# Optimization experiments

Measured on AMD Instinct MI355X. Metric: run time of the kernel, lower is better.

The kernel has to match this reference:

```python
import jax, jax.numpy as jnp
from jax import lax
import numpy as np

B, L, M, D, K, STRIDE = 32, 32768, 32, 128, 16, 8


def setup_inputs() -> dict:
    key = jax.random.key(0)
    k1, k2, k3, k4 = jax.random.split(key, 4)
    x = jax.random.normal(k1, (B, L, M), dtype=jnp.float32)
    # sorted timestamps per sample, like torch.sort(rand*100)
    timestamps = jnp.sort(jax.random.uniform(k2, (B, L), dtype=jnp.float32) * 100.0, axis=1)
    fan_in = M * K
    bound = 1.0 / np.sqrt(fan_in)
    conv_w = jax.random.uniform(k3, (D, M, K), dtype=jnp.float32, minval=-bound, maxval=bound)
    conv_b = jax.random.uniform(k4, (D,), dtype=jnp.float32, minval=-bound, maxval=bound)
    return {"x": x, "timestamps": timestamps, "conv_w": conv_w, "conv_b": conv_b}


def reference(x, timestamps, conv_w, conv_b):
    # Conv1d patch embedding: x [B,L,M] -> NCL -> conv -> [B,P,D]
    patches = lax.conv_general_dilated(
        x.transpose(0, 2, 1), conv_w,
        window_strides=(STRIDE,), padding=[(0, 0)],
        dimension_numbers=("NCH", "OIH", "NCH"))
    patches = patches.transpose(0, 2, 1) + conv_b  # [B,P,D]
    P = patches.shape[1]

    # Per-patch median timestamp (padding=0 -> all windows full length K).
    # torch.median on even-length returns the LOWER median = sorted idx (K-1)//2.
    starts = jnp.arange(P) * STRIDE
    idx = starts[:, None] + jnp.arange(K)          # [P,K]
    windows = timestamps[:, idx]                   # [B,P,K]
    med = jnp.sort(windows, axis=-1)[..., (K - 1) // 2]  # [B,P]

    # Sinusoidal PE at continuous times.
    div_term = jnp.exp(jnp.arange(0, D, 2).astype(jnp.float32) * (-np.log(10000.0) / D))
    ang = med[..., None] * div_term                # [B,P,D//2]
    pe = jnp.stack([jnp.sin(ang), jnp.cos(ang)], axis=-1).reshape(med.shape[0], P, D)
    return patches + pe
```

## Files before the change

kernel.cpp:

```cpp
#include <hip/hip_runtime.h>
#include <hip/hip_bf16.h>

#define Bn 32
#define Ln 32768
#define Mn 32
#define Dn 128
#define Pn 4095
#define KKn 512

typedef short  bf16x8 __attribute__((ext_vector_type(8)));
typedef float  f32x4  __attribute__((ext_vector_type(4)));

union BU { bf16x8 v; unsigned short u[8]; };

static __device__ __forceinline__ unsigned short f2bf(float f) {
  __hip_bfloat16 h = __float2bfloat16(f);
  return *reinterpret_cast<unsigned short*>(&h);
}

static __device__ __forceinline__ int swz(int g) {
  return (g & ~7) | ((g & 7) ^ ((g >> 5) & 7));
}

__global__ __launch_bounds__(256) void prep_w_kernel(const float* __restrict__ w,
                                                     unsigned short* __restrict__ wswz) {
  int idx = blockIdx.x * 256 + threadIdx.x;
  int j = idx & 7;
  int d = (idx >> 3) & 127;
  int g = idx >> 10;
  int kk = g * 8 + j;
  int k = kk >> 5;
  int m = kk & 31;
  wswz[idx] = f2bf(w[(d << 9) + (m << 4) + k]);
}

__global__ __launch_bounds__(256, 4) void gemm_pe_kernel(
    const float* __restrict__ x,
    const float* __restrict__ ts,
    const unsigned short* __restrict__ wswz,
    const float* __restrict__ bias,
    float* __restrict__ out) {

  __shared__ unsigned short xs[2080 * 8];
  __shared__ float tsl[64];

  const int b   = blockIdx.y;
  const int pt0 = blockIdx.x;
  const int tid = threadIdx.x;
  const int lane = tid & 63;
  const int wv   = tid >> 6;
  const int mrow = lane & 15;
  const int quad = lane >> 4;

  const float* xsrc = x + (size_t)b * Ln * Mn + (size_t)pt0 * 512 * Mn;
  const int r0 = pt0 * 512;

  float4 f[8][2];
  #pragma unroll
  for (int i = 0; i < 8; ++i) {
    int g = i * 256 + tid;
    const float4* src = reinterpret_cast<const float4*>(xsrc) + (size_t)g * 2;
    f[i][0] = src[0];
    f[i][1] = src[1];
  }
  float4 t0 = make_float4(0.f, 0.f, 0.f, 0.f), t1 = t0;
  if (tid < 32 && pt0 < 63) {
    const float4* src = reinterpret_cast<const float4*>(xsrc) + (size_t)(2048 + tid) * 2;
    t0 = src[0];
    t1 = src[1];
  }
  float tsv = 0.f;
  if (tid >= 64 && tid < 128)
    tsv = ts[(size_t)b * Ln + r0 + (tid - 64) * 8 + 7];
  const unsigned short* bbase = wswz + (((quad << 7) + (wv << 5) + mrow) << 3);
  bf16x8 bp[3][2];
  #pragma unroll
  for (int j = 0; j < 3; ++j) {
    bp[j][0] = *reinterpret_cast<const bf16x8*>(bbase + j * 4096);
    bp[j][1] = *reinterpret_cast<const bf16x8*>(bbase + 128 + j * 4096);
  }
  const int d0 = wv * 32 + mrow;
  const float NEG_C = -0.14391156831212810f;
  const float div0 = __expf(NEG_C * (float)(d0 >> 1));
  const float div1 = __expf(NEG_C * (float)((d0 + 16) >> 1));
  const float phs  = (d0 & 1) ? 1.5707963267948966f : 0.0f;
  const float bias0 = bias[d0];
  const float bias1 = bias[d0 + 16];

  __builtin_amdgcn_sched_barrier(0);

  #pragma unroll
  for (int i = 0; i < 8; ++i) {
    int g = i * 256 + tid;
    BU bu;
    bu.u[0] = f2bf(f[i][0].x); bu.u[1] = f2bf(f[i][0].y);
    bu.u[2] = f2bf(f[i][0].z); bu.u[3] = f2bf(f[i][0].w);
    bu.u[4] = f2bf(f[i][1].x); bu.u[5] = f2bf(f[i][1].y);
    bu.u[6] = f2bf(f[i][1].z); bu.u[7] = f2bf(f[i][1].w);
    *reinterpret_cast<bf16x8*>(&xs[swz(g) * 8]) = bu.v;
  }
  if (tid < 32) {
    BU bu;
    bu.u[0] = f2bf(t0.x); bu.u[1] = f2bf(t0.y); bu.u[2] = f2bf(t0.z); bu.u[3] = f2bf(t0.w);
    bu.u[4] = f2bf(t1.x); bu.u[5] = f2bf(t1.y); bu.u[6] = f2bf(t1.z); bu.u[7] = f2bf(t1.w);
    *reinterpret_cast<bf16x8*>(&xs[swz(2048 + tid) * 8]) = bu.v;
  }
  if (tid >= 64 && tid < 128) tsl[tid - 64] = tsv;
  __syncthreads();

  int agbase[4];
  #pragma unroll
  for (int pt = 0; pt < 4; ++pt) agbase[pt] = (pt * 16 + mrow) * 32 + quad;

  f32x4 acc[4][2] = {};

  bf16x8 a_cur[4];
  #pragma unroll
  for (int pt = 0; pt < 4; ++pt)
    a_cur[pt] = *reinterpret_cast<const bf16x8*>(&xs[swz(agbase[pt]) * 8]);

  #pragma unroll
  for (int t = 0; t < 16; ++t) {
    const int cur = t % 3;
    bf16x8 a_nxt[4];
    if (t < 15) {
      #pragma unroll
      for (int pt = 0; pt < 4; ++pt)
        a_nxt[pt] = *reinterpret_cast<const bf16x8*>(&xs[swz(agbase[pt] + (t + 1) * 4) * 8]);
    }
    bf16x8 bc0 = bp[cur][0], bc1 = bp[cur][1];
    if (t < 13) {
      bp[cur][0] = *reinterpret_cast<const bf16x8*>(bbase + (t + 3) * 4096);
      bp[cur][1] = *reinterpret_cast<const bf16x8*>(bbase + 128 + (t + 3) * 4096);
    }
    #pragma unroll
    for (int pt = 0; pt < 4; ++pt) {
      acc[pt][0] = __builtin_amdgcn_mfma_f32_16x16x32_bf16(a_cur[pt], bc0, acc[pt][0], 0, 0, 0);
      acc[pt][1] = __builtin_amdgcn_mfma_f32_16x16x32_bf16(a_cur[pt], bc1, acc[pt][1], 0, 0, 0);
    }
    if (t < 15) {
      #pragma unroll
      for (int pt = 0; pt < 4; ++pt) a_cur[pt] = a_nxt[pt];
    }
  }

  #pragma unroll
  for (int pt = 0; pt < 4; ++pt) {
    const int plbase = pt * 16 + quad * 4;
    f32x4 med4 = *reinterpret_cast<const f32x4*>(&tsl[plbase]);
    const int pbase = pt0 * 64 + plbase;
    float* obase = out + ((size_t)b * Pn + pbase) * Dn + d0;
    #pragma unroll
    for (int reg = 0; reg < 4; ++reg) {
      if (pbase + reg < Pn) {
        float m = med4[reg];
        float pe0 = __sinf(m * div0 + phs);
        float pe1 = __sinf(m * div1 + phs);
        obase[reg * Dn]      = acc[pt][0][reg] + bias0 + pe0;
        obase[reg * Dn + 16] = acc[pt][1][reg] + bias1 + pe1;
      }
    }
  }
}

extern "C" void kernel_launch(void* const* d_in, const int* in_sizes, int n_in,
                              void* d_out, int out_size, void* d_ws, size_t ws_size,
                              hipStream_t stream) {
  const float* x      = (const float*)d_in[0];
  const float* ts     = (const float*)d_in[1];
  const float* conv_w = (const float*)d_in[2];
  const float* conv_b = (const float*)d_in[3];
  float* out = (float*)d_out;
  unsigned short* wswz = (unsigned short*)d_ws;

  prep_w_kernel<<<256, 256, 0, stream>>>(conv_w, wswz);
  gemm_pe_kernel<<<dim3(64, Bn), 256, 0, stream>>>(x, ts, wswz, conv_b, out);
}
```

Before: 223.1 us.

## Process four 32-patch chunks per block with double-buffered LDS prefetch

Each block now handles 128 patches, split into four sub-tiles of 32. The next chunk of x is loaded into registers while the current chunk's MFMA work and output stores run, and it is written into an alternate LDS buffer. This halves the grid and overlaps global loads with compute and stores, aiming to hide memory latency. In exchange each block does more serial work and there are fewer blocks to spread across CUs, and weight fragments are reloaded every chunk.

```diff
diff --git a/kernel.cpp b/kernel.cpp
--- a/kernel.cpp
+++ b/kernel.cpp
@@ -34,6 +34,9 @@
   wswz[idx] = f2bf(w[(d << 9) + (m << 4) + k]);
 }
 
+#define GHALF 1056
+#define BUFS  (GHALF * 8)
+
 __global__ __launch_bounds__(256, 4) void gemm_pe_kernel(
     const float* __restrict__ x,
     const float* __restrict__ ts,
@@ -41,44 +44,46 @@
     const float* __restrict__ bias,
     float* __restrict__ out) {
 
-  __shared__ unsigned short xs[2080 * 8];
-  __shared__ float tsl[64];
-
-  const int b   = blockIdx.y;
-  const int pt0 = blockIdx.x;
-  const int tid = threadIdx.x;
+  __shared__ unsigned short xs[2][BUFS];
+  __shared__ float tsl[128];
+
+  const int b    = blockIdx.y;
+  const int pair = blockIdx.x;
+  const int tid  = threadIdx.x;
   const int lane = tid & 63;
   const int wv   = tid >> 6;
   const int mrow = lane & 15;
   const int quad = lane >> 4;
 
-  const float* xsrc = x + (size_t)b * Ln * Mn + (size_t)pt0 * 512 * Mn;
-  const int r0 = pt0 * 512;
-
-  float4 f[8][2];
+  const float* xpair = x + (size_t)b * Ln * Mn + (size_t)pair * 1024 * Mn;
+
+  float4 fr[5][2];
+  {
+    const float4* hsrc = reinterpret_cast<const float4*>(xpair);
+    #pragma unroll
+    for (int i = 0; i < 4; ++i) {
+      const float4* src = hsrc + (size_t)(i * 256 + tid) * 2;
+      fr[i][0] = src[0];
+      fr[i][1] = src[1];
+    }
+    fr[4][0] = make_float4(0.f, 0.f, 0.f, 0.f); fr[4][1] = fr[4][0];
+    if (tid < 32) {
+      const float4* src = hsrc + (size_t)(1024 + tid) * 2;
+      fr[4][0] = src[0];
+      fr[4][1] = src[1];
+    }
+  }
+  float tsv = 0.f;
+  if (tid < 128) tsv = ts[(size_t)b * Ln + (size_t)(pair * 128 + tid) * 8 + 7];
+
+  const unsigned short* bbase = wswz + (((quad << 7) + (wv << 5) + mrow) << 3);
+  bf16x8 bp[4][2];
   #pragma unroll
-  for (int i = 0; i < 8; ++i) {
-    int g = i * 256 + tid;
-    const float4* src = reinterpret_cast<const float4*>(xsrc) + (size_t)g * 2;
-    f[i][0] = src[0];
-    f[i][1] = src[1];
-  }
-  float4 t0 = make_float4(0.f, 0.f, 0.f, 0.f), t1 = t0;
-  if (tid < 32 && pt0 < 63) {
-    const float4* src = reinterpret_cast<const float4*>(xsrc) + (size_t)(2048 + tid) * 2;
-    t0 = src[0];
-    t1 = src[1];
-  }
-  float tsv = 0.f;
-  if (tid >= 64 && tid < 128)
-    tsv = ts[(size_t)b * Ln + r0 + (tid - 64) * 8 + 7];
-  const unsigned short* bbase = wswz + (((quad << 7) + (wv << 5) + mrow) << 3);
-  bf16x8 bp[3][2];
-  #pragma unroll
-  for (int j = 0; j < 3; ++j) {
+  for (int j = 0; j < 4; ++j) {
     bp[j][0] = *reinterpret_cast<const bf16x8*>(bbase + j * 4096);
     bp[j][1] = *reinterpret_cast<const bf16x8*>(bbase + 128 + j * 4096);
   }
+
   const int d0 = wv * 32 + mrow;
   const float NEG_C = -0.14391156831212810f;
   const float div0 = __expf(NEG_C * (float)(d0 >> 1));
@@ -90,75 +95,103 @@
   __builtin_amdgcn_sched_barrier(0);
 
   #pragma unroll
-  for (int i = 0; i < 8; ++i) {
-    int g = i * 256 + tid;
+  for (int i = 0; i < 4; ++i) {
+    int gl = i * 256 + tid;
     BU bu;
-    bu.u[0] = f2bf(f[i][0].x); bu.u[1] = f2bf(f[i][0].y);
-    bu.u[2] = f2bf(f[i][0].z); bu.u[3] = f2bf(f[i][0].w);
-    bu.u[4] = f2bf(f[i][1].x); bu.u[5] = f2bf(f[i][1].y);
-    bu.u[6] = f2bf(f[i][1].z); bu.u[7] = f2bf(f[i][1].w);
-    *reinterpret_cast<bf16x8*>(&xs[swz(g) * 8]) = bu.v;
+    bu.u[0] = f2bf(fr[i][0].x); bu.u[1] = f2bf(fr[i][0].y);
+    bu.u[2] = f2bf(fr[i][0].z); bu.u[3] = f2bf(fr[i][0].w);
+    bu.u[4] = f2bf(fr[i][1].x); bu.u[5] = f2bf(fr[i][1].y);
+    bu.u[6] = f2bf(fr[i][1].z); bu.u[7] = f2bf(fr[i][1].w);
+    *reinterpret_cast<bf16x8*>(&xs[0][swz(gl) * 8]) = bu.v;
   }
   if (tid < 32) {
     BU bu;
-    bu.u[0] = f2bf(t0.x); bu.u[1] = f2bf(t0.y); bu.u[2] = f2bf(t0.z); bu.u[3] = f2bf(t0.w);
-    bu.u[4] = f2bf(t1.x); bu.u[5] = f2bf(t1.y); bu.u[6] = f2bf(t1.z); bu.u[7] = f2bf(t1.w);
-    *reinterpret_cast<bf16x8*>(&xs[swz(2048 + tid) * 8]) = bu.v;
-  }
-  if (tid >= 64 && tid < 128) tsl[tid - 64] = tsv;
+    bu.u[0] = f2bf(fr[4][0].x); bu.u[1] = f2bf(fr[4][0].y);
+    bu.u[2] = f2bf(fr[4][0].z); bu.u[3] = f2bf(fr[4][0].w);
+    bu.u[4] = f2bf(fr[4][1].x); bu.u[5] = f2bf(fr[4][1].y);
+    bu.u[6] = f2bf(fr[4][1].z); bu.u[7] = f2bf(fr[4][1].w);
+    *reinterpret_cast<bf16x8*>(&xs[0][swz(1024 + tid) * 8]) = bu.v;
+  }
+  if (tid < 128) tsl[tid] = tsv;
   __syncthreads();
 
-  int agbase[4];
-  #pragma unroll
-  for (int pt = 0; pt < 4; ++pt) agbase[pt] = (pt * 16 + mrow) * 32 + quad;
-
-  f32x4 acc[4][2] = {};
-
-  bf16x8 a_cur[4];
-  #pragma unroll
-  for (int pt = 0; pt < 4; ++pt)
-    a_cur[pt] = *reinterpret_cast<const bf16x8*>(&xs[swz(agbase[pt]) * 8]);
-
-  #pragma unroll
-  for (int t = 0; t < 16; ++t) {
-    const int cur = t % 3;
-    bf16x8 a_nxt[4];
-    if (t < 15) {
+  const int agA = (mrow * 32) + quad;
+  const int agB = ((16 + mrow) * 32) + quad;
+
+  #pragma unroll 1
+  for (int h = 0; h < 4; ++h) {
+    if (h < 3) {
+      const float4* hsrc = reinterpret_cast<const float4*>(xpair + (size_t)(h + 1) * 8192);
       #pragma unroll
-      for (int pt = 0; pt < 4; ++pt)
-        a_nxt[pt] = *reinterpret_cast<const bf16x8*>(&xs[swz(agbase[pt] + (t + 1) * 4) * 8]);
-    }
-    bf16x8 bc0 = bp[cur][0], bc1 = bp[cur][1];
-    if (t < 13) {
-      bp[cur][0] = *reinterpret_cast<const bf16x8*>(bbase + (t + 3) * 4096);
-      bp[cur][1] = *reinterpret_cast<const bf16x8*>(bbase + 128 + (t + 3) * 4096);
-    }
+      for (int i = 0; i < 4; ++i) {
+        const float4* src = hsrc + (size_t)(i * 256 + tid) * 2;
+        fr[i][0] = src[0];
+        fr[i][1] = src[1];
+      }
+      fr[4][0] = make_float4(0.f, 0.f, 0.f, 0.f); fr[4][1] = fr[4][0];
+      if (tid < 32 && (pair * 1024 + (h + 1) * 256 + 256) < Ln) {
+        const float4* src = hsrc + (size_t)(1024 + tid) * 2;
+        fr[4][0] = src[0];
+        fr[4][1] = src[1];
+      }
+    }
+    __builtin_amdgcn_sched_barrier(0);
+
+    const unsigned short* xb = &xs[h & 1][0];
+    f32x4 acc[2][2] = {};
     #pragma unroll
-    for (int pt = 0; pt < 4; ++pt) {
-      acc[pt][0] = __builtin_amdgcn_mfma_f32_16x16x32_bf16(a_cur[pt], bc0, acc[pt][0], 0, 0, 0);
-      acc[pt][1] = __builtin_amdgcn_mfma_f32_16x16x32_bf16(a_cur[pt], bc1, acc[pt][1], 0, 0, 0);
-    }
-    if (t < 15) {
+    for (int t = 0; t < 16; ++t) {
+      bf16x8 a0 = *reinterpret_cast<const bf16x8*>(&xb[swz(agA + t * 4) * 8]);
+      bf16x8 a1 = *reinterpret_cast<const bf16x8*>(&xb[swz(agB + t * 4) * 8]);
+      const int cur = t & 3;
+      bf16x8 bc0 = bp[cur][0], bc1 = bp[cur][1];
+      bp[cur][0] = *reinterpret_cast<const bf16x8*>(bbase + ((t + 4) & 15) * 4096);
+      bp[cur][1] = *reinterpret_cast<const bf16x8*>(bbase + 128 + ((t + 4) & 15) * 4096);
+      acc[0][0] = __builtin_amdgcn_mfma_f32_16x16x32_bf16(a0, bc0, acc[0][0], 0, 0, 0);
+      acc[0][1] = __builtin_amdgcn_mfma_f32_16x16x32_bf16(a0, bc1, acc[0][1], 0, 0, 0);
+      acc[1][0] = __builtin_amdgcn_mfma_f32_16x16x32_bf16(a1, bc0, acc[1][0], 0, 0, 0);
+      acc[1][1] = __builtin_amdgcn_mfma_f32_16x16x32_bf16(a1, bc1, acc[1][1], 0, 0, 0);
+    }
+
+    #pragma unroll
+    for (int pt = 0; pt < 2; ++pt) {
+      const int plb = pt * 16 + quad * 4;
+      f32x4 med4 = *reinterpret_cast<const f32x4*>(&tsl[h * 32 + plb]);
+      const int pg = pair * 128 + h * 32 + plb;
+      float* obase = out + ((size_t)b * Pn + pg) * Dn + d0;
       #pragma unroll
-      for (int pt = 0; pt < 4; ++pt) a_cur[pt] = a_nxt[pt];
-    }
-  }
-
-  #pragma unroll
-  for (int pt = 0; pt < 4; ++pt) {
-    const int plbase = pt * 16 + quad * 4;
-    f32x4 med4 = *reinterpret_cast<const f32x4*>(&tsl[plbase]);
-    const int pbase = pt0 * 64 + plbase;
-    float* obase = out + ((size_t)b * Pn + pbase) * Dn + d0;
-    #pragma unroll
-    for (int reg = 0; reg < 4; ++reg) {
-      if (pbase + reg < Pn) {
-        float m = med4[reg];
-        float pe0 = __sinf(m * div0 + phs);
-        float pe1 = __sinf(m * div1 + phs);
-        obase[reg * Dn]      = acc[pt][0][reg] + bias0 + pe0;
-        obase[reg * Dn + 16] = acc[pt][1][reg] + bias1 + pe1;
-      }
+      for (int reg = 0; reg < 4; ++reg) {
+        if (pg + reg < Pn) {
+          float m = med4[reg];
+          float pe0 = __sinf(m * div0 + phs);
+          float pe1 = __sinf(m * div1 + phs);
+          obase[reg * Dn]      = acc[pt][0][reg] + bias0 + pe0;
+          obase[reg * Dn + 16] = acc[pt][1][reg] + bias1 + pe1;
+        }
+      }
+    }
+
+    if (h < 3) {
+      unsigned short* xw = &xs[(h + 1) & 1][0];
+      #pragma unroll
+      for (int i = 0; i < 4; ++i) {
+        int gl = i * 256 + tid;
+        BU bu;
+        bu.u[0] = f2bf(fr[i][0].x); bu.u[1] = f2bf(fr[i][0].y);
+        bu.u[2] = f2bf(fr[i][0].z); bu.u[3] = f2bf(fr[i][0].w);
+        bu.u[4] = f2bf(fr[i][1].x); bu.u[5] = f2bf(fr[i][1].y);
+        bu.u[6] = f2bf(fr[i][1].z); bu.u[7] = f2bf(fr[i][1].w);
+        *reinterpret_cast<bf16x8*>(&xw[swz(gl) * 8]) = bu.v;
+      }
+      if (tid < 32) {
+        BU bu;
+        bu.u[0] = f2bf(fr[4][0].x); bu.u[1] = f2bf(fr[4][0].y);
+        bu.u[2] = f2bf(fr[4][0].z); bu.u[3] = f2bf(fr[4][0].w);
+        bu.u[4] = f2bf(fr[4][1].x); bu.u[5] = f2bf(fr[4][1].y);
+        bu.u[6] = f2bf(fr[4][1].z); bu.u[7] = f2bf(fr[4][1].w);
+        *reinterpret_cast<bf16x8*>(&xw[swz(1024 + tid) * 8]) = bu.v;
+      }
+      __syncthreads();
     }
   }
 }
@@ -174,5 +207,5 @@
   unsigned short* wswz = (unsigned short*)d_ws;
 
   prep_w_kernel<<<256, 256, 0, stream>>>(conv_w, wswz);
-  gemm_pe_kernel<<<dim3(64, Bn), 256, 0, stream>>>(x, ts, wswz, conv_b, out);
-}
+  gemm_pe_kernel<<<dim3(32, Bn), 256, 0, stream>>>(x, ts, wswz, conv_b, out);
+}
```

Result: slower. 360.9 us (+61.8%).

## Stream x via direct global-to-LDS loads with double-buffered persistent tile loop

Applied to the files above, without the earlier changes.

Each block now handles 128 patches in 8 sub-tiles and double-buffers fp32 input rows in LDS using global_load_lds, prefetching the next sub-tile while the current one is computed. The fp32-to-bf16 conversion moves from the staging phase into the MFMA inner loop, and the weight fragments are kept in a rotating register ring of 8. The aim is to overlap global loads with compute and avoid routing x through registers, at the cost of half as many blocks, a sync per sub-tile, and conversion work repeated for each MFMA operand.

```diff
diff --git a/kernel.cpp b/kernel.cpp
--- a/kernel.cpp
+++ b/kernel.cpp
@@ -6,7 +6,6 @@
 #define Mn 32
 #define Dn 128
 #define Pn 4095
-#define KKn 512
 
 typedef short  bf16x8 __attribute__((ext_vector_type(8)));
 typedef float  f32x4  __attribute__((ext_vector_type(4)));
@@ -18,8 +17,10 @@
   return *reinterpret_cast<unsigned short*>(&h);
 }
 
-static __device__ __forceinline__ int swz(int g) {
-  return (g & ~7) | ((g & 7) ^ ((g >> 5) & 7));
+static __device__ __forceinline__ void gload_lds16(const void* g, void* l) {
+  __builtin_amdgcn_global_load_lds(
+      (const __attribute__((address_space(1))) unsigned int*)g,
+      (__attribute__((address_space(3))) unsigned int*)l, 16, 0, 0);
 }
 
 __global__ __launch_bounds__(256) void prep_w_kernel(const float* __restrict__ w,
@@ -34,6 +35,10 @@
   wswz[idx] = f2bf(w[(d << 9) + (m << 4) + k]);
 }
 
+#define QROWS 136
+#define QGRAN 1088
+#define QFLOAT (QGRAN * 4)
+
 __global__ __launch_bounds__(256, 4) void gemm_pe_kernel(
     const float* __restrict__ x,
     const float* __restrict__ ts,
@@ -41,44 +46,29 @@
     const float* __restrict__ bias,
     float* __restrict__ out) {
 
-  __shared__ unsigned short xs[2080 * 8];
-  __shared__ float tsl[64];
+  __shared__ float xsf[2][QFLOAT];
+  __shared__ float tsl[128];
 
-  const int b   = blockIdx.y;
-  const int pt0 = blockIdx.x;
-  const int tid = threadIdx.x;
+  const int b    = blockIdx.y;
+  const int pair = blockIdx.x;
+  const int tid  = threadIdx.x;
   const int lane = tid & 63;
   const int wv   = tid >> 6;
   const int mrow = lane & 15;
   const int quad = lane >> 4;
 
-  const float* xsrc = x + (size_t)b * Ln * Mn + (size_t)pt0 * 512 * Mn;
-  const int r0 = pt0 * 512;
+  const float* xb0 = x + (size_t)b * Ln * Mn;
 
-  float4 f[8][2];
+  const unsigned short* bbase = wswz + (((quad << 7) + (wv << 5) + mrow) << 3);
+  bf16x8 bp[8][2];
   #pragma unroll
-  for (int i = 0; i < 8; ++i) {
-    int g = i * 256 + tid;
-    const float4* src = reinterpret_cast<const float4*>(xsrc) + (size_t)g * 2;
-    f[i][0] = src[0];
-    f[i][1] = src[1];
-  }
-  float4 t0 = make_float4(0.f, 0.f, 0.f, 0.f), t1 = t0;
-  if (tid < 32 && pt0 < 63) {
-    const float4* src = reinterpret_cast<const float4*>(xsrc) + (size_t)(2048 + tid) * 2;
-    t0 = src[0];
-    t1 = src[1];
-  }
-  float tsv = 0.f;
-  if (tid >= 64 && tid < 128)
-    tsv = ts[(size_t)b * Ln + r0 + (tid - 64) * 8 + 7];
-  const unsigned short* bbase = wswz + (((quad << 7) + (wv << 5) + mrow) << 3);
-  bf16x8 bp[3][2];
-  #pragma unroll
-  for (int j = 0; j < 3; ++j) {
+  for (int j = 0; j < 8; ++j) {
     bp[j][0] = *reinterpret_cast<const bf16x8*>(bbase + j * 4096);
     bp[j][1] = *reinterpret_cast<const bf16x8*>(bbase + 128 + j * 4096);
   }
+
+  if (tid < 128) tsl[tid] = ts[(size_t)b * Ln + (size_t)(pair * 128 + tid) * 8 + 7];
+
   const int d0 = wv * 32 + mrow;
   const float NEG_C = -0.14391156831212810f;
   const float div0 = __expf(NEG_C * (float)(d0 >> 1));
@@ -87,80 +77,75 @@
   const float bias0 = bias[d0];
   const float bias1 = bias[d0 + 16];
 
-  __builtin_amdgcn_sched_barrier(0);
+#define STAGE(qq, bf)                                                          \
+  do {                                                                         \
+    const int grow = pair * 1024 + (qq) * 128;                                 \
+    const char* gsrc = (const char*)(xb0 + (size_t)grow * 32);                 \
+    _Pragma("unroll")                                                          \
+    for (int i = 0; i < 4; ++i) {                                              \
+      int s = i * 256 + tid;                                                   \
+      int r = s >> 3, c = s & 7;                                               \
+      int sg = (r << 3) + (c ^ ((r >> 3) & 7));                                \
+      gload_lds16(gsrc + (size_t)sg * 16,                                      \
+                  (void*)&xsf[bf][(size_t)(i * 256 + wv * 64) * 4]);           \
+    }                                                                          \
+    if (tid < 64 && grow + QROWS <= Ln) {              \
+      int s = 1024 + tid;                                                      \
+      int r = s >> 3, c = s & 7;                                               \
+      int sg = (r << 3) + (c ^ ((r >> 3) & 7));                                \
+      gload_lds16(gsrc + (size_t)sg * 16, (void*)&xsf[bf][1024 * 4]);          \
+    }                                                                          \
+  } while (0)
 
-  #pragma unroll
-  for (int i = 0; i < 8; ++i) {
-    int g = i * 256 + tid;
-    BU bu;
-    bu.u[0] = f2bf(f[i][0].x); bu.u[1] = f2bf(f[i][0].y);
-    bu.u[2] = f2bf(f[i][0].z); bu.u[3] = f2bf(f[i][0].w);
-    bu.u[4] = f2bf(f[i][1].x); bu.u[5] = f2bf(f[i][1].y);
-    bu.u[6] = f2bf(f[i][1].z); bu.u[7] = f2bf(f[i][1].w);
-    *reinterpret_cast<bf16x8*>(&xs[swz(g) * 8]) = bu.v;
-  }
-  if (tid < 32) {
-    BU bu;
-    bu.u[0] = f2bf(t0.x); bu.u[1] = f2bf(t0.y); bu.u[2] = f2bf(t0.z); bu.u[3] = f2bf(t0.w);
-    bu.u[4] = f2bf(t1.x); bu.u[5] = f2bf(t1.y); bu.u[6] = f2bf(t1.z); bu.u[7] = f2bf(t1.w);
-    *reinterpret_cast<bf16x8*>(&xs[swz(2048 + tid) * 8]) = bu.v;
-  }
-  if (tid >= 64 && tid < 128) tsl[tid - 64] = tsv;
+  STAGE(0, 0);
   __syncthreads();
 
-  int agbase[4];
-  #pragma unroll
-  for (int pt = 0; pt < 4; ++pt) agbase[pt] = (pt * 16 + mrow) * 32 + quad;
+  #pragma unroll 1
+  for (int q = 0; q < 8; ++q) {
+    if (q < 7) STAGE(q + 1, (q + 1) & 1);
+    __builtin_amdgcn_sched_barrier(0);
 
-  f32x4 acc[4][2] = {};
+    const float* xbuf = xsf[q & 1];
+    f32x4 acc0 = {0.f, 0.f, 0.f, 0.f};
+    f32x4 acc1 = {0.f, 0.f, 0.f, 0.f};
+    #pragma unroll
+    for (int t = 0; t < 16; ++t) {
+      const int rl = (mrow << 3) + t;
+      const int sw = (rl >> 3) & 7;
+      const int c0 = (quad << 1) ^ sw;
+      f32x4 af0 = *reinterpret_cast<const f32x4*>(&xbuf[(size_t)((rl << 3) + c0) * 4]);
+      f32x4 af1 = *reinterpret_cast<const f32x4*>(&xbuf[(size_t)((rl << 3) + (c0 ^ 1)) * 4]);
+      BU bu;
+      bu.u[0] = f2bf(af0[0]); bu.u[1] = f2bf(af0[1]);
+      bu.u[2] = f2bf(af0[2]); bu.u[3] = f2bf(af0[3]);
+      bu.u[4] = f2bf(af1[0]); bu.u[5] = f2bf(af1[1]);
+      bu.u[6] = f2bf(af1[2]); bu.u[7] = f2bf(af1[3]);
+      const int cur = t & 7;
+      bf16x8 bc0 = bp[cur][0], bc1 = bp[cur][1];
+      bp[cur][0] = *reinterpret_cast<const bf16x8*>(bbase + ((t + 8) & 15) * 4096);
+      bp[cur][1] = *reinterpret_cast<const bf16x8*>(bbase + 128 + ((t + 8) & 15) * 4096);
+      acc0 = __builtin_amdgcn_mfma_f32_16x16x32_bf16(bu.v, bc0, acc0, 0, 0, 0);
+      acc1 = __builtin_amdgcn_mfma_f32_16x16x32_bf16(bu.v, bc1, acc1, 0, 0, 0);
+    }
 
-  bf16x8 a_cur[4];
-  #pragma unroll
-  for (int pt = 0; pt < 4; ++pt)
-    a_cur[pt] = *reinterpret_cast<const bf16x8*>(&xs[swz(agbase[pt]) * 8]);
-
-  #pragma unroll
-  for (int t = 0; t < 16; ++t) {
-    const int cur = t % 3;
-    bf16x8 a_nxt[4];
-    if (t < 15) {
+    {
+      const int plb = quad * 4;
+      f32x4 med4 = *reinterpret_cast<const f32x4*>(&tsl[q * 16 + plb]);
+      const int pg = pair * 128 + q * 16 + plb;
+      float* obase = out + ((size_t)b * Pn + pg) * Dn + d0;
       #pragma unroll
-      for (int pt = 0; pt < 4; ++pt)
-        a_nxt[pt] = *reinterpret_cast<const bf16x8*>(&xs[swz(agbase[pt] + (t + 1) * 4) * 8]);
-    }
-    bf16x8 bc0 = bp[cur][0], bc1 = bp[cur][1];
-    if (t < 13) {
-      bp[cur][0] = *reinterpret_cast<const bf16x8*>(bbase + (t + 3) * 4096);
-      bp[cur][1] = *reinterpret_cast<const bf16x8*>(bbase + 128 + (t + 3) * 4096);
-    }
-    #pragma unroll
-    for (int pt = 0; pt < 4; ++pt) {
-      acc[pt][0] = __builtin_amdgcn_mfma_f32_16x16x32_bf16(a_cur[pt], bc0, acc[pt][0], 0, 0, 0);
-      acc[pt][1] = __builtin_amdgcn_mfma_f32_16x16x32_bf16(a_cur[pt], bc1, acc[pt][1], 0, 0, 0);
-    }
-    if (t < 15) {
-      #pragma unroll
-      for (int pt = 0; pt < 4; ++pt) a_cur[pt] = a_nxt[pt];
-    }
-  }
-
-  #pragma unroll
-  for (int pt = 0; pt < 4; ++pt) {
-    const int plbase = pt * 16 + quad * 4;
-    f32x4 med4 = *reinterpret_cast<const f32x4*>(&tsl[plbase]);
-    const int pbase = pt0 * 64 + plbase;
-    float* obase = out + ((size_t)b * Pn + pbase) * Dn + d0;
-    #pragma unroll
-    for (int reg = 0; reg < 4; ++reg) {
-      if (pbase + reg < Pn) {
-        float m = med4[reg];
-        float pe0 = __sinf(m * div0 + phs);
-        float pe1 = __sinf(m * div1 + phs);
-        obase[reg * Dn]      = acc[pt][0][reg] + bias0 + pe0;
-        obase[reg * Dn + 16] = acc[pt][1][reg] + bias1 + pe1;
+      for (int reg = 0; reg < 4; ++reg) {
+        if (pg + reg < Pn) {
+          float m = med4[reg];
+          obase[reg * Dn]      = acc0[reg] + bias0 + __sinf(m * div0 + phs);
+          obase[reg * Dn + 16] = acc1[reg] + bias1 + __sinf(m * div1 + phs);
+        }
       }
     }
+
+    __syncthreads();
   }
+#undef STAGE
 }
 
 extern "C" void kernel_launch(void* const* d_in, const int* in_sizes, int n_in,
@@ -174,5 +159,5 @@
   unsigned short* wswz = (unsigned short*)d_ws;
 
   prep_w_kernel<<<256, 256, 0, stream>>>(conv_w, wswz);
-  gemm_pe_kernel<<<dim3(64, Bn), 256, 0, stream>>>(x, ts, wswz, conv_b, out);
+  gemm_pe_kernel<<<dim3(32, Bn), 256, 0, stream>>>(x, ts, wswz, conv_b, out);
 }
```

Result: slower. 385.6 us (+72.9%).
